# Optimization experiments

Measured on AMD Instinct MI355X. Metric: run time of the kernel, lower is better.

The kernel has to match this reference:

```python
import jax, jax.numpy as jnp
import numpy as np

D = 64      # d_model == initialFeatureSize
H = 8       # n_heads
F2 = D + 2  # hidden_size + 2


def _ln(x, g, b):
    m = x.mean(-1, keepdims=True)
    v = ((x - m) ** 2).mean(-1, keepdims=True)
    return (x - m) / jnp.sqrt(v + 1e-5) * g + b


def _mask_weights(idx):
    # softmax of where(idx>0, 1, -9e15) along axis 1 -> mean over non-pad slots
    return jax.nn.softmax(jnp.where(idx > 0, 1.0, -9e15), axis=1)


def _tblock(x, mask, qkv, Wo, bo, ln, ffW, ffb):
    # standard masked multi-head self-attention block (eval mode, dropout off)
    B, L, Dm = x.shape
    dh = Dm // H
    q = (x @ qkv[0]).reshape(B, L, H, dh)
    k = (x @ qkv[1]).reshape(B, L, H, dh)
    v = (x @ qkv[2]).reshape(B, L, H, dh)
    s = jnp.einsum('blhd,bmhd->bhlm', q, k) / jnp.sqrt(jnp.asarray(dh, x.dtype))
    s = jnp.where(mask[:, None, None, :], -1e9, s)
    ctx = jnp.einsum('bhlm,bmhd->blhd', jax.nn.softmax(s, -1), v).reshape(B, L, Dm)
    x = _ln(x + ctx @ Wo + bo, ln[0, 0], ln[0, 1])
    ff = jax.nn.relu(x @ ffW[0] + ffb[0]) @ ffW[1] + ffb[1]
    return _ln(x + ff, ln[1, 0], ln[1, 1])


def _forward(user_emb, global_cen_emb, local_time_emb, cas_pos_emb, local_inf_emb,
             hgnn_w1, hgnn_w2, hgnn_w3, text_lin_W, text_lin_b,
             weight, weight2, fus_l1_W, fus_l1_b, fus_l2_W, fus_l2_b, out_W, out_b,
             tb_qkv, tb_Wo, tb_bo, tb_ln, tb_ff_W, tb_ff_b,
             text2emb, spread_status,
             data_idx, seq, timestamps, user_level, useq, user_inf, user_cen):
    # --- dead code kept for faithfulness (result unused) ---
    w3n = hgnn_w3 / jnp.linalg.norm(hgnn_w3, axis=1, keepdims=True)
    _tw = (w3n @ w3n.T).mean()
    t = text2emb @ text_lin_W + text_lin_b
    _t = ((t - t.min()) / (t.max() - t.min()) * 999).astype(jnp.int32)
    # --- HGNN layer: gather -> masked mean -> relu -> gather -> masked mean ---
    x = (user_emb + global_cen_emb[user_cen]) @ hgnn_w1            # [N, D]
    edge = jax.nn.relu(jnp.einsum('nlc,nl->nc', x[seq], _mask_weights(seq)))  # [E, D]
    node = jnp.einsum('umc,um->uc', (edge @ hgnn_w2)[useq], _mask_weights(useq))  # [N, D]
    # --- batch gather for attention branches ---
    seq_b = seq[data_idx]                                          # [B, L]
    w_b = _mask_weights(seq_b)
    att_mask = seq_b == 0                                          # PAD == 0
    adj = node[seq_b]                                              # [B, L, D]
    # temporal branch
    h_t = adj + local_time_emb[timestamps[data_idx]]
    o_t = _tblock(h_t, att_mask, tb_qkv[0], tb_Wo[0], tb_bo[0], tb_ln[0], tb_ff_W[0], tb_ff_b[0])
    n_t = jnp.einsum('blc,bl->bc', o_t, w_b)
    n_t = jnp.concatenate([n_t, spread_status[data_idx][:, 2:] / 3600.0 / 24.0], -1) @ weight
    # structural branch
    h_s = adj + local_inf_emb[user_inf[data_idx]] + cas_pos_emb[user_level[data_idx]]
    o_s = _tblock(h_s, att_mask, tb_qkv[1], tb_Wo[1], tb_bo[1], tb_ln[1], tb_ff_W[1], tb_ff_b[1])
    n_s = jnp.einsum('blc,bl->bc', o_s, w_b)
    n_s = jnp.concatenate([n_s, spread_status[data_idx][:, :2]], -1) @ weight2
    # gated fusion
    emb = jnp.stack([n_t, n_s])                                    # [2, B, F2]
    score = jax.nn.softmax(jnp.tanh(emb @ fus_l1_W + fus_l1_b) @ fus_l2_W + fus_l2_b, axis=0)
    fused = (score * emb).sum(0)
    return jax.nn.log_softmax(fused @ out_W + out_b, axis=1)       # [B, 2]


def setup_inputs() -> dict:
    key = jax.random.key(0)
    ks = iter(jax.random.split(key, 48))
    N, E, L, M, B, EMB = 100000, 20000, 50, 20, 1024, 300
    stdv = 1.0 / np.sqrt(D)
    u = lambda shape: jax.random.uniform(next(ks), shape, jnp.float32, -stdv, stdv)
    ri = lambda shape, hi: jax.random.randint(next(ks), shape, 0, hi, jnp.int32)
    ln_init = jnp.broadcast_to(jnp.stack([jnp.ones(D), jnp.zeros(D)])[None, None], (2, 2, 2, D))
    return dict(
        user_emb=u((N, D)), global_cen_emb=u((600, D)), local_time_emb=u((5000, D)),
        cas_pos_emb=u((50, D)), local_inf_emb=u((200, D)),
        hgnn_w1=u((D, D)), hgnn_w2=u((D, D)), hgnn_w3=u((100, EMB)),
        text_lin_W=u((EMB, 200)), text_lin_b=u((200,)),
        weight=u((F2, F2)), weight2=u((F2, F2)),
        fus_l1_W=u((F2, F2)), fus_l1_b=u((F2,)), fus_l2_W=u((F2, 1)), fus_l2_b=u((1,)),
        out_W=u((F2, 2)), out_b=u((2,)),
        tb_qkv=u((2, 3, D, D)), tb_Wo=u((2, D, D)), tb_bo=u((2, D)),
        tb_ln=jnp.array(ln_init),
        tb_ff_W=u((2, 2, D, D)), tb_ff_b=u((2, 2, D)),
        text2emb=jax.random.normal(next(ks), (E, EMB), jnp.float32),
        spread_status=jax.random.uniform(next(ks), (E, 4), jnp.float32, 0.0, 100.0),
        data_idx=ri((B,), E), seq=ri((E, L), N), timestamps=ri((E, L), 5000),
        user_level=ri((E, L), 50), useq=ri((N, M), E), user_inf=ri((E, L), 200),
        user_cen=ri((N,), 600),
    )


def reference(user_emb, global_cen_emb, local_time_emb, cas_pos_emb, local_inf_emb,
              hgnn_w1, hgnn_w2, hgnn_w3, text_lin_W, text_lin_b,
              weight, weight2, fus_l1_W, fus_l1_b, fus_l2_W, fus_l2_b, out_W, out_b,
              tb_qkv, tb_Wo, tb_bo, tb_ln, tb_ff_W, tb_ff_b,
              text2emb, spread_status,
              data_idx, seq, timestamps, user_level, useq, user_inf, user_cen):
    return _forward(user_emb, global_cen_emb, local_time_emb, cas_pos_emb, local_inf_emb,
                    hgnn_w1, hgnn_w2, hgnn_w3, text_lin_W, text_lin_b,
                    weight, weight2, fus_l1_W, fus_l1_b, fus_l2_W, fus_l2_b, out_W, out_b,
                    tb_qkv, tb_Wo, tb_bo, tb_ln, tb_ff_W, tb_ff_b,
                    text2emb, spread_status,
                    data_idx, seq, timestamps, user_level, useq, user_inf, user_cen)
```

## Files before the change

kernel.cpp:

```cpp
#include <hip/hip_runtime.h>
#include <hip/hip_bf16.h>

#define D  64
#define L  50
#define M  20
#define BB 1024
#define F2 66
#define NEDGE 20000
#define NUSER 100000

typedef __attribute__((ext_vector_type(8))) short bf16x8;
typedef __attribute__((ext_vector_type(4))) float f32x4;

#define MFMA(a,b,c) __builtin_amdgcn_mfma_f32_16x16x32_bf16(a,b,c,0,0,0)

__device__ __forceinline__ short f2bf(float f) {
    union { __hip_bfloat16 h; unsigned short u; } cv;
    cv.h = __float2bfloat16(f);
    return (short)cv.u;
}
__device__ __forceinline__ uint32_t pk2(float a, float b) {
    union { __hip_bfloat162 h; uint32_t u; } cv;
    cv.h.x = __float2bfloat16(a);
    cv.h.y = __float2bfloat16(b);
    return cv.u;
}
__device__ __forceinline__ float bf2f(short s) {
    return __uint_as_float(((uint32_t)(unsigned short)s) << 16);
}
__device__ __forceinline__ float bf2fu(unsigned short s) {
    return __uint_as_float(((uint32_t)s) << 16);
}
__device__ __forceinline__ int swz(int row, int col) {
    return row * 64 + (col ^ ((row & 7) << 3));
}
__device__ __forceinline__ float wsum(float v) {
    #pragma unroll
    for (int off = 32; off > 0; off >>= 1) v += __shfl_xor(v, off);
    return v;
}


__global__ __launch_bounds__(256) void k_prep(
    const float* __restrict__ qkv, const float* __restrict__ Wo,
    const float* __restrict__ ffW, const float* __restrict__ w2,
    const float* __restrict__ w1, short* __restrict__ wb)
{
    int idx = blockIdx.x * 256 + threadIdx.x;
    int mat = idx >> 12, e = idx & 4095;
    int c = e >> 6, k = e & 63;
    const float* src;
    if (mat == 13)      src = w1;
    else if (mat == 12) src = w2;
    else {
        int bi = mat / 6, m = mat % 6;
        if (m < 3)       src = qkv + ((size_t)bi * 3 + m) * 4096;
        else if (m == 3) src = Wo + (size_t)bi * 4096;
        else             src = ffW + ((size_t)bi * 2 + (m - 4)) * 4096;
    }
    wb[(size_t)mat * 4096 + c * 64 + k] = f2bf(src[k * 64 + c]);
}


__global__ __launch_bounds__(256) void k_hgnn1m(
    const float* __restrict__ user_emb, const float* __restrict__ cen_emb,
    const int* __restrict__ user_cen, const short* __restrict__ w1t,
    unsigned short* __restrict__ xb)
{
    const int tid = threadIdx.x, lane = tid & 63, lo = lane & 15, hg = lane >> 4, w = tid >> 6;
    const int row0 = blockIdx.x * 64 + 16 * w;
    const int arow = row0 + lo;
    const bool av = arow < NUSER;
    const int cidx = av ? user_cen[arow] : 0;

    f32x4 acc[4];
    #pragma unroll
    for (int c = 0; c < 4; ++c) { acc[c][0] = acc[c][1] = acc[c][2] = acc[c][3] = 0.f; }

    #pragma unroll
    for (int ks = 0; ks < 2; ++ks) {
        bf16x8 a;
        if (av) {
            const float4 u0 = *(const float4*)&user_emb[(size_t)arow * 64 + 32 * ks + 8 * hg];
            const float4 u1 = *(const float4*)&user_emb[(size_t)arow * 64 + 32 * ks + 8 * hg + 4];
            const float4 c0 = *(const float4*)&cen_emb[(size_t)cidx * 64 + 32 * ks + 8 * hg];
            const float4 c1 = *(const float4*)&cen_emb[(size_t)cidx * 64 + 32 * ks + 8 * hg + 4];
            uint32_t p0 = pk2(u0.x + c0.x, u0.y + c0.y);
            uint32_t p1 = pk2(u0.z + c0.z, u0.w + c0.w);
            uint32_t p2 = pk2(u1.x + c1.x, u1.y + c1.y);
            uint32_t p3 = pk2(u1.z + c1.z, u1.w + c1.w);
            union { uint32_t u[4]; bf16x8 v; } af;
            af.u[0] = p0; af.u[1] = p1; af.u[2] = p2; af.u[3] = p3;
            a = af.v;
        } else {
            #pragma unroll
            for (int i = 0; i < 8; ++i) a[i] = 0;
        }
        #pragma unroll
        for (int c = 0; c < 4; ++c) {
            bf16x8 bb = *(const bf16x8*)(w1t + (16 * c + lo) * 64 + 32 * ks + 8 * hg);
            acc[c] = MFMA(a, bb, acc[c]);
        }
    }
    #pragma unroll
    for (int c = 0; c < 4; ++c) {
        #pragma unroll
        for (int r = 0; r < 4; ++r) {
            int row = row0 + 4 * hg + r;
            if (row < NUSER) xb[(size_t)row * 64 + 16 * c + lo] = (unsigned short)f2bf(acc[c][r]);
        }
    }
}


__global__ __launch_bounds__(256) void k_edge_gather(
    const unsigned short* __restrict__ xb, const int* __restrict__ seq,
    unsigned short* __restrict__ em)
{
    const int j = threadIdx.x & 63;
    const int e = blockIdx.x * 4 + (threadIdx.x >> 6);
    int my = (j < L) ? seq[(size_t)e * L + j] : 0;
    int cnt = (int)__popcll(__ballot(j < L && my > 0));
    float wv = cnt ? 1.f / (float)cnt : 1.f / (float)L;
    unsigned short tv[50];
    #pragma unroll
    for (int l = 0; l < 50; ++l) tv[l] = xb[(size_t)__shfl(my, l) * D + j];
    float ss[4] = {0.f, 0.f, 0.f, 0.f};
    #pragma unroll
    for (int l = 0; l < 50; ++l) {
        int idx = __shfl(my, l);
        bool use = cnt ? (idx > 0) : true;
        ss[l & 3] += use ? bf2fu(tv[l]) : 0.f;
    }
    float m = fmaxf(((ss[0] + ss[1]) + (ss[2] + ss[3])) * wv, 0.f);
    em[(size_t)e * D + j] = (unsigned short)f2bf(m);
}


__global__ __launch_bounds__(256) void k_gemm_edge(
    const unsigned short* __restrict__ em, const short* __restrict__ w2t,
    unsigned short* __restrict__ e2b)
{
    const int tid = threadIdx.x, lane = tid & 63, lo = lane & 15, hg = lane >> 4, w = tid >> 6;
    const int row0 = blockIdx.x * 64 + 16 * w;
    bf16x8 zf;
    #pragma unroll
    for (int i = 0; i < 8; ++i) zf[i] = 0;
    f32x4 acc[4];
    #pragma unroll
    for (int c = 0; c < 4; ++c) { acc[c][0] = acc[c][1] = acc[c][2] = acc[c][3] = 0.f; }
    #pragma unroll
    for (int ks = 0; ks < 2; ++ks) {
        bf16x8 a = zf;
        if (row0 + lo < NEDGE)
            a = *(const bf16x8*)&em[(size_t)(row0 + lo) * D + 32 * ks + 8 * hg];
        #pragma unroll
        for (int c = 0; c < 4; ++c) {
            bf16x8 bb = *(const bf16x8*)(w2t + (16 * c + lo) * 64 + 32 * ks + 8 * hg);
            acc[c] = MFMA(a, bb, acc[c]);
        }
    }
    #pragma unroll
    for (int c = 0; c < 4; ++c) {
        #pragma unroll
        for (int r = 0; r < 4; ++r) {
            int row = row0 + 4 * hg + r;
            if (row < NEDGE) e2b[(size_t)row * D + 16 * c + lo] = (unsigned short)f2bf(acc[c][r]);
        }
    }
}


__global__ __launch_bounds__(256) void k_nodem(
    const unsigned short* __restrict__ e2b, const int* __restrict__ seq,
    const int* __restrict__ useq, const int* __restrict__ data_idx,
    unsigned short* __restrict__ nb)
{
    const int j = threadIdx.x & 63;
    const int w = threadIdx.x >> 6;
    const int p = blockIdx.x * 4 + w;
    const int b = p / L, l = p - b * L;
    const int ib = data_idx[b];
    const int u = seq[(size_t)ib * L + l];
    int my = (j < M) ? useq[(size_t)u * M + j] : 0;
    int cnt = (int)__popcll(__ballot(j < M && my > 0));
    float wv = cnt ? 1.f / (float)cnt : 1.f / (float)M;
    unsigned short tv[20];
    #pragma unroll
    for (int m = 0; m < M; ++m) tv[m] = e2b[(size_t)__shfl(my, m) * D + j];
    float ss[4] = {0.f, 0.f, 0.f, 0.f};
    #pragma unroll
    for (int m = 0; m < M; ++m) {
        int q = __shfl(my, m);
        bool use = cnt ? (q > 0) : true;
        ss[m & 3] += use ? bf2fu(tv[m]) : 0.f;
    }
    float acc = ((ss[0] + ss[1]) + (ss[2] + ss[3])) * wv;
    nb[(size_t)p * D + j] = (unsigned short)f2bf(acc);
}

#define XB 0
#define QB 3328
#define KB 6656
#define VBT 9984

__global__ __launch_bounds__(512) void k_tblock2(
    const unsigned short* __restrict__ nb,
    const int* __restrict__ seq, const int* __restrict__ data_idx,
    const int* __restrict__ timestamps, const int* __restrict__ user_inf,
    const int* __restrict__ user_level,
    const float* __restrict__ time_emb, const float* __restrict__ inf_emb,
    const float* __restrict__ pos_emb,
    const short* __restrict__ wb,
    const float* __restrict__ bo_all, const float* __restrict__ ln_all,
    const float* __restrict__ ffb_all, const float* __restrict__ spread,
    const float* __restrict__ weight, const float* __restrict__ weight2,
    float* __restrict__ n_t, float* __restrict__ n_s)
{
    const int tid = threadIdx.x;
    const int lane = tid & 63, lo = lane & 15, hg = lane >> 4, w = tid >> 6;
    const int branch = blockIdx.x & 1, b = blockIdx.x >> 1;
    const int ib = data_idx[b];

    const short* WT  = wb + (size_t)branch * 6 * 4096;
    const float* bo  = bo_all + branch * 64;
    const float* lnp = ln_all + branch * 256;
    const float* ffb = ffb_all + branch * 128;
    const float* Wbr = branch ? weight2 : weight;
    float* nout      = branch ? n_s : n_t;
    const int eoff   = branch ? 0 : 2;
    const float escale = branch ? 1.f : (1.f / 86400.f);

    __shared__ __align__(16) short sm[14080];
    __shared__ float nbuf[4][64];
    __shared__ float nvec[F2];
    __shared__ int   seqi[52];

    for (int i = tid; i < 1600; i += 512) {
        int row = i >> 5, cp = (i & 31) * 2;
        uint32_t nn = *(const uint32_t*)(nb + (size_t)b * 3200 + row * 64 + cp);
        float h0 = bf2fu((unsigned short)(nn & 0xffff));
        float h1 = bf2fu((unsigned short)(nn >> 16));
        if (branch == 0) {
            int ts = timestamps[(size_t)ib * L + row];
            float2 te = *(const float2*)(time_emb + (size_t)ts * 64 + cp);
            h0 += te.x; h1 += te.y;
        } else {
            int inf = user_inf[(size_t)ib * L + row];
            int lev = user_level[(size_t)ib * L + row];
            float2 ie = *(const float2*)(inf_emb + (size_t)inf * 64 + cp);
            float2 pe = *(const float2*)(pos_emb + (size_t)lev * 64 + cp);
            h0 += ie.x + pe.x; h1 += ie.y + pe.y;
        }
        *(uint32_t*)&sm[XB + swz(row, cp)] = pk2(h0, h1);
    }
    if (tid < 52) seqi[tid] = (tid < 50) ? seq[(size_t)ib * L + tid] : 0;
    {
        const int zb0 = XB + 50 * 64, zb1 = QB + 50 * 64, zb2 = KB + 50 * 64;
        for (int i = tid; i < 448; i += 512) {
            ((int*)(sm + zb0))[i] = 0;
            ((int*)(sm + zb1))[i] = 0;
            ((int*)(sm + zb2))[i] = 0;
        }
    }
    __syncthreads();

    #pragma unroll
    for (int t2 = 0; t2 < 2; ++t2) {
        int task = w + 8 * t2;
        if (task < 12) {
            int mat = task >> 2, rt = task & 3;
            f32x4 a4[4];
            #pragma unroll
            for (int c = 0; c < 4; ++c) { a4[c][0] = a4[c][1] = a4[c][2] = a4[c][3] = 0.f; }
            #pragma unroll
            for (int ks = 0; ks < 2; ++ks) {
                bf16x8 xa = *(const bf16x8*)&sm[XB + swz(16 * rt + lo, 32 * ks + 8 * hg)];
                #pragma unroll
                for (int c = 0; c < 4; ++c) {
                    bf16x8 bb = *(const bf16x8*)(WT + (size_t)mat * 4096 +
                                                 (16 * c + lo) * 64 + 32 * ks + 8 * hg);
                    a4[c] = MFMA(xa, bb, a4[c]);
                }
            }
            if (mat == 0) {
                #pragma unroll
                for (int c = 0; c < 4; ++c)
                    #pragma unroll
                    for (int r = 0; r < 4; ++r) {
                        int row = 16 * rt + 4 * hg + r;
                        if (row < 52)
                            sm[QB + swz(row, 16 * c + lo)] = f2bf(a4[c][r] * 0.35355339059327378f);
                    }
            } else if (mat == 1) {
                #pragma unroll
                for (int c = 0; c < 4; ++c)
                    #pragma unroll
                    for (int r = 0; r < 4; ++r) {
                        int row = 16 * rt + 4 * hg + r;
                        if (row < 52) sm[KB + swz(row, 16 * c + lo)] = f2bf(a4[c][r]);
                    }
            } else {
                #pragma unroll
                for (int c = 0; c < 4; ++c)
                    #pragma unroll
                    for (int r = 0; r < 4; ++r) {
                        int row = 16 * rt + 4 * hg + r, col = 16 * c + lo;
                        sm[VBT + swz(col, row)] = (row < 50) ? f2bf(a4[c][r]) : (short)0;
                    }
            }
        }
    }
    __syncthreads();

    int svl = (lane < 50) ? seqi[lane] : 0;
    int cnt = (int)__popcll(__ballot(svl > 0));
    float msel[4][4];
    #pragma unroll
    for (int mt = 0; mt < 4; ++mt) {
        #pragma unroll
        for (int r = 0; r < 4; ++r) {
            int m = 16 * mt + 4 * hg + r;
            msel[mt][r] = (m < 50) ? ((seqi[m] > 0) ? 0.f : -1e9f) : -3.0e38f;
        }
    }

    bf16x8 zf;
    #pragma unroll
    for (int i = 0; i < 8; ++i) zf[i] = 0;

    f32x4 ctx[4];
    {
        int hd = w;
        bf16x8 ka[4], qf[4];
        #pragma unroll
        for (int t = 0; t < 4; ++t) {
            ka[t] = zf; qf[t] = zf;
            if (hg == 0) {
                ka[t] = *(const bf16x8*)&sm[KB + swz(16 * t + lo, hd * 8)];
                qf[t] = *(const bf16x8*)&sm[QB + swz(16 * t + lo, hd * 8)];
            }
        }
        f32x4 s[4][4];
        #pragma unroll
        for (int mt = 0; mt < 4; ++mt) {
            #pragma unroll
            for (int c = 0; c < 4; ++c) {
                f32x4 z; z[0] = z[1] = z[2] = z[3] = 0.f;
                s[mt][c] = MFMA(ka[mt], qf[c], z);
            }
        }
        #pragma unroll
        for (int mt = 0; mt < 4; ++mt) {
            #pragma unroll
            for (int r = 0; r < 4; ++r) {
                float ms = msel[mt][r];
                bool valid = (ms == 0.f);
                #pragma unroll
                for (int c = 0; c < 4; ++c) s[mt][c][r] = valid ? s[mt][c][r] : ms;
            }
        }
        uint32_t pk[4][4][2];
        #pragma unroll
        for (int c = 0; c < 4; ++c) {
            float mx = -3.4e38f;
            #pragma unroll
            for (int mt = 0; mt < 4; ++mt) {
                #pragma unroll
                for (int r = 0; r < 4; ++r) mx = fmaxf(mx, s[mt][c][r]);
            }
            mx = fmaxf(mx, __shfl_xor(mx, 16));
            mx = fmaxf(mx, __shfl_xor(mx, 32));
            float den = 0.f;
            #pragma unroll
            for (int mt = 0; mt < 4; ++mt) {
                #pragma unroll
                for (int r = 0; r < 4; ++r) {
                    float e = __expf(s[mt][c][r] - mx);
                    s[mt][c][r] = e; den += e;
                }
            }
            den += __shfl_xor(den, 16);
            den += __shfl_xor(den, 32);
            float inv = 1.f / den;
            #pragma unroll
            for (int mt = 0; mt < 4; ++mt) {
                pk[mt][c][0] = pk2(s[mt][c][0] * inv, s[mt][c][1] * inv);
                pk[mt][c][1] = pk2(s[mt][c][2] * inv, s[mt][c][3] * inv);
            }
        }
        #pragma unroll
        for (int t = 0; t < 4; ++t) { ctx[t][0] = ctx[t][1] = ctx[t][2] = ctx[t][3] = 0.f; }
        #pragma unroll
        for (int rt = 0; rt < 4; ++rt) {
            #pragma unroll
            for (int ks = 0; ks < 2; ++ks) {
                union { uint32_t u[4]; bf16x8 v; } af;
                #pragma unroll
                for (int j = 0; j < 4; ++j) {
                    int src = lo + 16 * (2 * (hg & 1) + (j >> 1));
                    uint32_t a0 = __shfl(pk[2 * ks][rt][j & 1], src);
                    uint32_t a1 = __shfl(pk[2 * ks + 1][rt][j & 1], src);
                    af.u[j] = (hg < 2) ? a0 : a1;
                }
                bf16x8 bfr = zf;
                if (lo < 8) bfr = *(const bf16x8*)&sm[VBT + swz(hd * 8 + lo, 32 * ks + 8 * hg)];
                ctx[rt] = MFMA(af.v, bfr, ctx[rt]);
            }
        }
    }
    __syncthreads();
    if (lo < 8) {
        #pragma unroll
        for (int rt = 0; rt < 4; ++rt) {
            #pragma unroll
            for (int r = 0; r < 4; ++r) {
                int row = 16 * rt + 4 * hg + r;
                if (row < 52) sm[KB + swz(row, w * 8 + lo)] = f2bf(ctx[rt][r]);
            }
        }
    }
    __syncthreads();

    if (w < 4) {
        float g1[4], b1[4], g2[4], b2[4], boc[4], f1b[4], f2b[4];
        #pragma unroll
        for (int c = 0; c < 4; ++c) {
            int col = 16 * c + lo;
            g1[c] = lnp[col];        b1[c] = lnp[64 + col];
            g2[c] = lnp[128 + col];  b2[c] = lnp[192 + col];
            boc[c] = bo[col]; f1b[c] = ffb[col]; f2b[c] = ffb[64 + col];
        }

        f32x4 acc[4];
        #pragma unroll
        for (int c = 0; c < 4; ++c) { acc[c][0] = acc[c][1] = acc[c][2] = acc[c][3] = 0.f; }
        #pragma unroll
        for (int ks = 0; ks < 2; ++ks) {
            bf16x8 a = *(const bf16x8*)&sm[KB + swz(16 * w + lo, 32 * ks + 8 * hg)];
            #pragma unroll
            for (int c = 0; c < 4; ++c) {
                bf16x8 bb = *(const bf16x8*)(WT + 3 * 4096 + (16 * c + lo) * 64 + 32 * ks + 8 * hg);
                acc[c] = MFMA(a, bb, acc[c]);
            }
        }
        float x1v[4][4];
        #pragma unroll
        for (int r = 0; r < 4; ++r) {
            int row = 16 * w + 4 * hg + r;
            float t0 = bf2f(sm[XB + swz(row, lo)])      + acc[0][r] + boc[0];
            float t1 = bf2f(sm[XB + swz(row, 16 + lo)]) + acc[1][r] + boc[1];
            float t2 = bf2f(sm[XB + swz(row, 32 + lo)]) + acc[2][r] + boc[2];
            float t3 = bf2f(sm[XB + swz(row, 48 + lo)]) + acc[3][r] + boc[3];
            float s1 = t0 + t1 + t2 + t3;
            float q1 = t0 * t0 + t1 * t1 + t2 * t2 + t3 * t3;
            #pragma unroll
            for (int d = 1; d <= 8; d <<= 1) { s1 += __shfl_xor(s1, d); q1 += __shfl_xor(q1, d); }
            float mean = s1 * 0.015625f;
            float var = q1 * 0.015625f - mean * mean;
            float rin = rsqrtf(var + 1e-5f);
            float x0 = (t0 - mean) * rin * g1[0] + b1[0];
            float x1 = (t1 - mean) * rin * g1[1] + b1[1];
            float x2 = (t2 - mean) * rin * g1[2] + b1[2];
            float x3 = (t3 - mean) * rin * g1[3] + b1[3];
            x1v[0][r] = x0; x1v[1][r] = x1; x1v[2][r] = x2; x1v[3][r] = x3;
            if (row < 52) {
                sm[QB + swz(row, lo)]      = f2bf(x0);
                sm[QB + swz(row, 16 + lo)] = f2bf(x1);
                sm[QB + swz(row, 32 + lo)] = f2bf(x2);
                sm[QB + swz(row, 48 + lo)] = f2bf(x3);
            }
        }
        #pragma unroll
        for (int c = 0; c < 4; ++c) { acc[c][0] = acc[c][1] = acc[c][2] = acc[c][3] = 0.f; }
        #pragma unroll
        for (int ks = 0; ks < 2; ++ks) {
            bf16x8 a = *(const bf16x8*)&sm[QB + swz(16 * w + lo, 32 * ks + 8 * hg)];
            #pragma unroll
            for (int c = 0; c < 4; ++c) {
                bf16x8 bb = *(const bf16x8*)(WT + 4 * 4096 + (16 * c + lo) * 64 + 32 * ks + 8 * hg);
                acc[c] = MFMA(a, bb, acc[c]);
            }
        }
        #pragma unroll
        for (int c = 0; c < 4; ++c) {
            #pragma unroll
            for (int r = 0; r < 4; ++r) {
                int row = 16 * w + 4 * hg + r;
                if (row < 52) sm[KB + swz(row, 16 * c + lo)] = f2bf(fmaxf(acc[c][r] + f1b[c], 0.f));
            }
        }
        #pragma unroll
        for (int c = 0; c < 4; ++c) { acc[c][0] = acc[c][1] = acc[c][2] = acc[c][3] = 0.f; }
        #pragma unroll
        for (int ks = 0; ks < 2; ++ks) {
            bf16x8 a = *(const bf16x8*)&sm[KB + swz(16 * w + lo, 32 * ks + 8 * hg)];
            #pragma unroll
            for (int c = 0; c < 4; ++c) {
                bf16x8 bb = *(const bf16x8*)(WT + 5 * 4096 + (16 * c + lo) * 64 + 32 * ks + 8 * hg);
                acc[c] = MFMA(a, bb, acc[c]);
            }
        }
        float wv = (cnt > 0) ? 1.f / (float)cnt : 0.02f;
        float np[4] = {0.f, 0.f, 0.f, 0.f};
        #pragma unroll
        for (int r = 0; r < 4; ++r) {
            int row = 16 * w + 4 * hg + r;
            float t0 = x1v[0][r] + acc[0][r] + f2b[0];
            float t1 = x1v[1][r] + acc[1][r] + f2b[1];
            float t2 = x1v[2][r] + acc[2][r] + f2b[2];
            float t3 = x1v[3][r] + acc[3][r] + f2b[3];
            float s1 = t0 + t1 + t2 + t3;
            float q1 = t0 * t0 + t1 * t1 + t2 * t2 + t3 * t3;
            #pragma unroll
            for (int d = 1; d <= 8; d <<= 1) { s1 += __shfl_xor(s1, d); q1 += __shfl_xor(q1, d); }
            float mean = s1 * 0.015625f;
            float var = q1 * 0.015625f - mean * mean;
            float rin = rsqrtf(var + 1e-5f);
            float wl = 0.f;
            if (row < 50) {
                int sv = seqi[row];
                wl = (cnt > 0) ? ((sv > 0) ? wv : 0.f) : wv;
            }
            np[0] += ((t0 - mean) * rin * g2[0] + b2[0]) * wl;
            np[1] += ((t1 - mean) * rin * g2[1] + b2[1]) * wl;
            np[2] += ((t2 - mean) * rin * g2[2] + b2[2]) * wl;
            np[3] += ((t3 - mean) * rin * g2[3] + b2[3]) * wl;
        }
        #pragma unroll
        for (int c = 0; c < 4; ++c) {
            np[c] += __shfl_xor(np[c], 16);
            np[c] += __shfl_xor(np[c], 32);
        }
        if (hg == 0) {
            #pragma unroll
            for (int c = 0; c < 4; ++c) nbuf[w][16 * c + lo] = np[c];
        }
    }
    __syncthreads();
    if (tid < 64) nvec[tid] = nbuf[0][tid] + nbuf[1][tid] + nbuf[2][tid] + nbuf[3][tid];
    else if (tid == 64) nvec[64] = spread[(size_t)ib * 4 + eoff] * escale;
    else if (tid == 65) nvec[65] = spread[(size_t)ib * 4 + eoff + 1] * escale;
    __syncthreads();
    if (tid < F2) {
        float a = 0.f;
        for (int k = 0; k < F2; ++k) a += nvec[k] * Wbr[k * F2 + tid];
        nout[(size_t)b * F2 + tid] = a;
    }
}


__global__ __launch_bounds__(256) void k_fuse(
    const float* __restrict__ n_t, const float* __restrict__ n_s,
    const float* __restrict__ l1W, const float* __restrict__ l1b,
    const float* __restrict__ l2W, const float* __restrict__ l2b,
    const float* __restrict__ outW, const float* __restrict__ outb,
    float* __restrict__ out)
{
    const int w = threadIdx.x >> 6, j = threadIdx.x & 63;
    const int b = blockIdx.x * 4 + w;
    __shared__ float et[4][F2], es[4][F2], fused[4][F2];
    for (int t = j; t < F2; t += 64) { et[w][t] = n_t[(size_t)b * F2 + t]; es[w][t] = n_s[(size_t)b * F2 + t]; }
    float sl[2];
    for (int s = 0; s < 2; ++s) {
        const float* e = s ? es[w] : et[w];
        float part = 0.f;
        for (int t = j; t < F2; t += 64) {
            float acc = l1b[t];
            for (int k = 0; k < F2; ++k) acc += e[k] * l1W[k * F2 + t];
            part += tanhf(acc) * l2W[t];
        }
        part = wsum(part);
        sl[s] = part + l2b[0];
    }
    float mx = fmaxf(sl[0], sl[1]);
    float e0 = __expf(sl[0] - mx), e1 = __expf(sl[1] - mx);
    float inv = 1.f / (e0 + e1);
    float sc0 = e0 * inv, sc1 = e1 * inv;
    for (int t = j; t < F2; t += 64) fused[w][t] = sc0 * et[w][t] + sc1 * es[w][t];
    float p0 = 0.f, p1 = 0.f;
    for (int t = j; t < F2; t += 64) {
        p0 += fused[w][t] * outW[t * 2 + 0];
        p1 += fused[w][t] * outW[t * 2 + 1];
    }
    p0 = wsum(p0); p1 = wsum(p1);
    if (j == 0) {
        float l0 = p0 + outb[0], l1v = p1 + outb[1];
        float m = fmaxf(l0, l1v);
        float lse = m + logf(__expf(l0 - m) + __expf(l1v - m));
        out[(size_t)b * 2 + 0] = l0 - lse;
        out[(size_t)b * 2 + 1] = l1v - lse;
    }
}

extern "C" void kernel_launch(void* const* d_in, const int* in_sizes, int n_in,
                              void* d_out, int out_size, void* d_ws, size_t ws_size,
                              hipStream_t stream)
{
    (void)in_sizes; (void)n_in; (void)out_size; (void)ws_size;
    const float* user_emb = (const float*)d_in[0];
    const float* cen_emb  = (const float*)d_in[1];
    const float* time_emb = (const float*)d_in[2];
    const float* pos_emb  = (const float*)d_in[3];
    const float* inf_emb  = (const float*)d_in[4];
    const float* w1       = (const float*)d_in[5];
    const float* w2       = (const float*)d_in[6];
    const float* weight   = (const float*)d_in[10];
    const float* weight2  = (const float*)d_in[11];
    const float* l1W      = (const float*)d_in[12];
    const float* l1b      = (const float*)d_in[13];
    const float* l2W      = (const float*)d_in[14];
    const float* l2b      = (const float*)d_in[15];
    const float* outW     = (const float*)d_in[16];
    const float* outb     = (const float*)d_in[17];
    const float* qkv      = (const float*)d_in[18];
    const float* Wo       = (const float*)d_in[19];
    const float* bo       = (const float*)d_in[20];
    const float* lnp      = (const float*)d_in[21];
    const float* ffW      = (const float*)d_in[22];
    const float* ffb      = (const float*)d_in[23];
    const float* spread   = (const float*)d_in[25];
    const int* data_idx   = (const int*)d_in[26];
    const int* seq        = (const int*)d_in[27];
    const int* timestamps = (const int*)d_in[28];
    const int* user_level = (const int*)d_in[29];
    const int* useq       = (const int*)d_in[30];
    const int* user_inf   = (const int*)d_in[31];
    const int* user_cen   = (const int*)d_in[32];

    unsigned short* wbt = (unsigned short*)d_ws;
    unsigned short* xb  = wbt + 57344;
    unsigned short* em  = xb + 6400000;
    unsigned short* e2b = em + 1280000;
    unsigned short* nbm = e2b + 1280000;
    float* n_t = (float*)(nbm + 3276800);
    float* n_s = n_t + 67584;
    float* out = (float*)d_out;

    k_prep<<<224, 256, 0, stream>>>(qkv, Wo, ffW, w2, w1, (short*)wbt);
    k_hgnn1m<<<1563, 256, 0, stream>>>(user_emb, cen_emb, user_cen,
                                       (const short*)wbt + 13 * 4096, xb);
    k_edge_gather<<<5000, 256, 0, stream>>>(xb, seq, em);
    k_gemm_edge<<<313, 256, 0, stream>>>(em, (const short*)wbt + 12 * 4096, e2b);
    k_nodem<<<12800, 256, 0, stream>>>(e2b, seq, useq, data_idx, nbm);
    k_tblock2<<<2048, 512, 0, stream>>>(nbm, seq, data_idx, timestamps, user_inf,
                                        user_level, time_emb, inf_emb, pos_emb,
                                        (const short*)wbt, bo, lnp, ffb, spread,
                                        weight, weight2, n_t, n_s);
    k_fuse<<<256, 256, 0, stream>>>(n_t, n_s, l1W, l1b, l2W, l2b, outW, outb, out);
}
```

Before: 200.3 us.

## Process both transformer branches in one block per batch item

The transformer-block kernel now handles both the time and influence branches for one batch element in a single 512-thread block, not one block per branch. The shared nb row, seq indices and block setup are loaded once, and all 8 waves stay busy in the QKV and FFN stages, where the old per-branch layout left some waves idle. Shared memory per block doubles and each wave holds two context accumulators, which raises register pressure and may reduce occupancy even with the launch-bounds hint.

```diff
diff --git a/kernel.cpp b/kernel.cpp
--- a/kernel.cpp
+++ b/kernel.cpp
@@ -203,8 +203,9 @@
 #define QB 3328
 #define KB 6656
 #define VBT 9984
-
-__global__ __launch_bounds__(512) void k_tblock2(
+#define BRO 14080
+
+__global__ __launch_bounds__(512, 4) void k_tblock2(
     const unsigned short* __restrict__ nb,
     const int* __restrict__ seq, const int* __restrict__ data_idx,
     const int* __restrict__ timestamps, const int* __restrict__ user_inf,
@@ -219,96 +220,86 @@
 {
     const int tid = threadIdx.x;
     const int lane = tid & 63, lo = lane & 15, hg = lane >> 4, w = tid >> 6;
-    const int branch = blockIdx.x & 1, b = blockIdx.x >> 1;
+    const int b = blockIdx.x;
     const int ib = data_idx[b];
 
-    const short* WT  = wb + (size_t)branch * 6 * 4096;
-    const float* bo  = bo_all + branch * 64;
-    const float* lnp = ln_all + branch * 256;
-    const float* ffb = ffb_all + branch * 128;
-    const float* Wbr = branch ? weight2 : weight;
-    float* nout      = branch ? n_s : n_t;
-    const int eoff   = branch ? 0 : 2;
-    const float escale = branch ? 1.f : (1.f / 86400.f);
-
-    __shared__ __align__(16) short sm[14080];
-    __shared__ float nbuf[4][64];
-    __shared__ float nvec[F2];
+    __shared__ __align__(16) short sm[2 * BRO];
+    __shared__ float nbuf[2][4][64];
+    __shared__ float nvec[2][F2];
     __shared__ int   seqi[52];
 
     for (int i = tid; i < 1600; i += 512) {
         int row = i >> 5, cp = (i & 31) * 2;
         uint32_t nn = *(const uint32_t*)(nb + (size_t)b * 3200 + row * 64 + cp);
-        float h0 = bf2fu((unsigned short)(nn & 0xffff));
-        float h1 = bf2fu((unsigned short)(nn >> 16));
-        if (branch == 0) {
-            int ts = timestamps[(size_t)ib * L + row];
-            float2 te = *(const float2*)(time_emb + (size_t)ts * 64 + cp);
-            h0 += te.x; h1 += te.y;
-        } else {
-            int inf = user_inf[(size_t)ib * L + row];
-            int lev = user_level[(size_t)ib * L + row];
-            float2 ie = *(const float2*)(inf_emb + (size_t)inf * 64 + cp);
-            float2 pe = *(const float2*)(pos_emb + (size_t)lev * 64 + cp);
-            h0 += ie.x + pe.x; h1 += ie.y + pe.y;
-        }
-        *(uint32_t*)&sm[XB + swz(row, cp)] = pk2(h0, h1);
+        float n0 = bf2fu((unsigned short)(nn & 0xffff));
+        float n1 = bf2fu((unsigned short)(nn >> 16));
+        int ts  = timestamps[(size_t)ib * L + row];
+        int inf = user_inf[(size_t)ib * L + row];
+        int lev = user_level[(size_t)ib * L + row];
+        float2 te = *(const float2*)(time_emb + (size_t)ts * 64 + cp);
+        float2 ie = *(const float2*)(inf_emb + (size_t)inf * 64 + cp);
+        float2 pe = *(const float2*)(pos_emb + (size_t)lev * 64 + cp);
+        *(uint32_t*)&sm[XB + swz(row, cp)]       = pk2(n0 + te.x, n1 + te.y);
+        *(uint32_t*)&sm[BRO + XB + swz(row, cp)] = pk2(n0 + ie.x + pe.x, n1 + ie.y + pe.y);
     }
     if (tid < 52) seqi[tid] = (tid < 50) ? seq[(size_t)ib * L + tid] : 0;
     {
-        const int zb0 = XB + 50 * 64, zb1 = QB + 50 * 64, zb2 = KB + 50 * 64;
         for (int i = tid; i < 448; i += 512) {
-            ((int*)(sm + zb0))[i] = 0;
-            ((int*)(sm + zb1))[i] = 0;
-            ((int*)(sm + zb2))[i] = 0;
+            ((int*)(sm + XB + 50 * 64))[i] = 0;
+            ((int*)(sm + QB + 50 * 64))[i] = 0;
+            ((int*)(sm + KB + 50 * 64))[i] = 0;
+            ((int*)(sm + BRO + XB + 50 * 64))[i] = 0;
+            ((int*)(sm + BRO + QB + 50 * 64))[i] = 0;
+            ((int*)(sm + BRO + KB + 50 * 64))[i] = 0;
         }
     }
     __syncthreads();
 
     #pragma unroll
-    for (int t2 = 0; t2 < 2; ++t2) {
-        int task = w + 8 * t2;
-        if (task < 12) {
-            int mat = task >> 2, rt = task & 3;
-            f32x4 a4[4];
-            #pragma unroll
-            for (int c = 0; c < 4; ++c) { a4[c][0] = a4[c][1] = a4[c][2] = a4[c][3] = 0.f; }
-            #pragma unroll
-            for (int ks = 0; ks < 2; ++ks) {
-                bf16x8 xa = *(const bf16x8*)&sm[XB + swz(16 * rt + lo, 32 * ks + 8 * hg)];
-                #pragma unroll
-                for (int c = 0; c < 4; ++c) {
-                    bf16x8 bb = *(const bf16x8*)(WT + (size_t)mat * 4096 +
-                                                 (16 * c + lo) * 64 + 32 * ks + 8 * hg);
-                    a4[c] = MFMA(xa, bb, a4[c]);
+    for (int t3 = 0; t3 < 3; ++t3) {
+        int task = w + 8 * t3;
+        int br  = (task >= 12) ? 1 : 0;
+        int rem = task - 12 * br;
+        int mat = rem >> 2, rt = rem & 3;
+        const int RB = br * BRO;
+        const short* WTb = wb + (size_t)br * 6 * 4096 + (size_t)mat * 4096;
+        f32x4 a4[4];
+        #pragma unroll
+        for (int c = 0; c < 4; ++c) { a4[c][0] = a4[c][1] = a4[c][2] = a4[c][3] = 0.f; }
+        #pragma unroll
+        for (int ks = 0; ks < 2; ++ks) {
+            bf16x8 xa = *(const bf16x8*)&sm[RB + XB + swz(16 * rt + lo, 32 * ks + 8 * hg)];
+            #pragma unroll
+            for (int c = 0; c < 4; ++c) {
+                bf16x8 bb = *(const bf16x8*)(WTb + (16 * c + lo) * 64 + 32 * ks + 8 * hg);
+                a4[c] = MFMA(xa, bb, a4[c]);
+            }
+        }
+        if (mat == 0) {
+            #pragma unroll
+            for (int c = 0; c < 4; ++c)
+                #pragma unroll
+                for (int r = 0; r < 4; ++r) {
+                    int row = 16 * rt + 4 * hg + r;
+                    if (row < 52)
+                        sm[RB + QB + swz(row, 16 * c + lo)] = f2bf(a4[c][r] * 0.35355339059327378f);
                 }
-            }
-            if (mat == 0) {
-                #pragma unroll
-                for (int c = 0; c < 4; ++c)
-                    #pragma unroll
-                    for (int r = 0; r < 4; ++r) {
-                        int row = 16 * rt + 4 * hg + r;
-                        if (row < 52)
-                            sm[QB + swz(row, 16 * c + lo)] = f2bf(a4[c][r] * 0.35355339059327378f);
-                    }
-            } else if (mat == 1) {
-                #pragma unroll
-                for (int c = 0; c < 4; ++c)
-                    #pragma unroll
-                    for (int r = 0; r < 4; ++r) {
-                        int row = 16 * rt + 4 * hg + r;
-                        if (row < 52) sm[KB + swz(row, 16 * c + lo)] = f2bf(a4[c][r]);
-                    }
-            } else {
-                #pragma unroll
-                for (int c = 0; c < 4; ++c)
-                    #pragma unroll
-                    for (int r = 0; r < 4; ++r) {
-                        int row = 16 * rt + 4 * hg + r, col = 16 * c + lo;
-                        sm[VBT + swz(col, row)] = (row < 50) ? f2bf(a4[c][r]) : (short)0;
-                    }
-            }
+        } else if (mat == 1) {
+            #pragma unroll
+            for (int c = 0; c < 4; ++c)
+                #pragma unroll
+                for (int r = 0; r < 4; ++r) {
+                    int row = 16 * rt + 4 * hg + r;
+                    if (row < 52) sm[RB + KB + swz(row, 16 * c + lo)] = f2bf(a4[c][r]);
+                }
+        } else {
+            #pragma unroll
+            for (int c = 0; c < 4; ++c)
+                #pragma unroll
+                for (int r = 0; r < 4; ++r) {
+                    int row = 16 * rt + 4 * hg + r, col = 16 * c + lo;
+                    sm[RB + VBT + swz(col, row)] = (row < 50) ? f2bf(a4[c][r]) : (short)0;
+                }
         }
     }
     __syncthreads();
@@ -329,16 +320,18 @@
     #pragma unroll
     for (int i = 0; i < 8; ++i) zf[i] = 0;
 
-    f32x4 ctx[4];
-    {
-        int hd = w;
+    f32x4 ctx2[2][4];
+    const int hd = w;
+    #pragma unroll
+    for (int br = 0; br < 2; ++br) {
+        const int RB = br * BRO;
         bf16x8 ka[4], qf[4];
         #pragma unroll
         for (int t = 0; t < 4; ++t) {
             ka[t] = zf; qf[t] = zf;
             if (hg == 0) {
-                ka[t] = *(const bf16x8*)&sm[KB + swz(16 * t + lo, hd * 8)];
-                qf[t] = *(const bf16x8*)&sm[QB + swz(16 * t + lo, hd * 8)];
+                ka[t] = *(const bf16x8*)&sm[RB + KB + swz(16 * t + lo, hd * 8)];
+                qf[t] = *(const bf16x8*)&sm[RB + QB + swz(16 * t + lo, hd * 8)];
             }
         }
         f32x4 s[4][4];
@@ -390,7 +383,9 @@
             }
         }
         #pragma unroll
-        for (int t = 0; t < 4; ++t) { ctx[t][0] = ctx[t][1] = ctx[t][2] = ctx[t][3] = 0.f; }
+        for (int t = 0; t < 4; ++t) {
+            ctx2[br][t][0] = ctx2[br][t][1] = ctx2[br][t][2] = ctx2[br][t][3] = 0.f;
+        }
         #pragma unroll
         for (int rt = 0; rt < 4; ++rt) {
             #pragma unroll
@@ -404,25 +399,36 @@
                     af.u[j] = (hg < 2) ? a0 : a1;
                 }
                 bf16x8 bfr = zf;
-                if (lo < 8) bfr = *(const bf16x8*)&sm[VBT + swz(hd * 8 + lo, 32 * ks + 8 * hg)];
-                ctx[rt] = MFMA(af.v, bfr, ctx[rt]);
+                if (lo < 8) bfr = *(const bf16x8*)&sm[RB + VBT + swz(hd * 8 + lo, 32 * ks + 8 * hg)];
+                ctx2[br][rt] = MFMA(af.v, bfr, ctx2[br][rt]);
             }
         }
     }
     __syncthreads();
     if (lo < 8) {
         #pragma unroll
-        for (int rt = 0; rt < 4; ++rt) {
-            #pragma unroll
-            for (int r = 0; r < 4; ++r) {
-                int row = 16 * rt + 4 * hg + r;
-                if (row < 52) sm[KB + swz(row, w * 8 + lo)] = f2bf(ctx[rt][r]);
+        for (int br = 0; br < 2; ++br) {
+            const int RB = br * BRO;
+            #pragma unroll
+            for (int rt = 0; rt < 4; ++rt) {
+                #pragma unroll
+                for (int r = 0; r < 4; ++r) {
+                    int row = 16 * rt + 4 * hg + r;
+                    if (row < 52) sm[RB + KB + swz(row, hd * 8 + lo)] = f2bf(ctx2[br][rt][r]);
+                }
             }
         }
     }
     __syncthreads();
 
-    if (w < 4) {
+    {
+        const int ebr = w >> 2, ws = w & 3;
+        const int RB = ebr * BRO;
+        const short* WT  = wb + (size_t)ebr * 6 * 4096;
+        const float* bo  = bo_all + ebr * 64;
+        const float* lnp = ln_all + ebr * 256;
+        const float* ffb = ffb_all + ebr * 128;
+
         float g1[4], b1[4], g2[4], b2[4], boc[4], f1b[4], f2b[4];
         #pragma unroll
         for (int c = 0; c < 4; ++c) {
@@ -437,7 +443,7 @@
         for (int c = 0; c < 4; ++c) { acc[c][0] = acc[c][1] = acc[c][2] = acc[c][3] = 0.f; }
         #pragma unroll
         for (int ks = 0; ks < 2; ++ks) {
-            bf16x8 a = *(const bf16x8*)&sm[KB + swz(16 * w + lo, 32 * ks + 8 * hg)];
+            bf16x8 a = *(const bf16x8*)&sm[RB + KB + swz(16 * ws + lo, 32 * ks + 8 * hg)];
             #pragma unroll
             for (int c = 0; c < 4; ++c) {
                 bf16x8 bb = *(const bf16x8*)(WT + 3 * 4096 + (16 * c + lo) * 64 + 32 * ks + 8 * hg);
@@ -447,11 +453,11 @@
         float x1v[4][4];
         #pragma unroll
         for (int r = 0; r < 4; ++r) {
-            int row = 16 * w + 4 * hg + r;
-            float t0 = bf2f(sm[XB + swz(row, lo)])      + acc[0][r] + boc[0];
-            float t1 = bf2f(sm[XB + swz(row, 16 + lo)]) + acc[1][r] + boc[1];
-            float t2 = bf2f(sm[XB + swz(row, 32 + lo)]) + acc[2][r] + boc[2];
-            float t3 = bf2f(sm[XB + swz(row, 48 + lo)]) + acc[3][r] + boc[3];
+            int row = 16 * ws + 4 * hg + r;
+            float t0 = bf2f(sm[RB + XB + swz(row, lo)])      + acc[0][r] + boc[0];
+            float t1 = bf2f(sm[RB + XB + swz(row, 16 + lo)]) + acc[1][r] + boc[1];
+            float t2 = bf2f(sm[RB + XB + swz(row, 32 + lo)]) + acc[2][r] + boc[2];
+            float t3 = bf2f(sm[RB + XB + swz(row, 48 + lo)]) + acc[3][r] + boc[3];
             float s1 = t0 + t1 + t2 + t3;
             float q1 = t0 * t0 + t1 * t1 + t2 * t2 + t3 * t3;
             #pragma unroll
@@ -465,17 +471,17 @@
             float x3 = (t3 - mean) * rin * g1[3] + b1[3];
             x1v[0][r] = x0; x1v[1][r] = x1; x1v[2][r] = x2; x1v[3][r] = x3;
             if (row < 52) {
-                sm[QB + swz(row, lo)]      = f2bf(x0);
-                sm[QB + swz(row, 16 + lo)] = f2bf(x1);
-                sm[QB + swz(row, 32 + lo)] = f2bf(x2);
-                sm[QB + swz(row, 48 + lo)] = f2bf(x3);
+                sm[RB + QB + swz(row, lo)]      = f2bf(x0);
+                sm[RB + QB + swz(row, 16 + lo)] = f2bf(x1);
+                sm[RB + QB + swz(row, 32 + lo)] = f2bf(x2);
+                sm[RB + QB + swz(row, 48 + lo)] = f2bf(x3);
             }
         }
         #pragma unroll
         for (int c = 0; c < 4; ++c) { acc[c][0] = acc[c][1] = acc[c][2] = acc[c][3] = 0.f; }
         #pragma unroll
         for (int ks = 0; ks < 2; ++ks) {
-            bf16x8 a = *(const bf16x8*)&sm[QB + swz(16 * w + lo, 32 * ks + 8 * hg)];
+            bf16x8 a = *(const bf16x8*)&sm[RB + QB + swz(16 * ws + lo, 32 * ks + 8 * hg)];
             #pragma unroll
             for (int c = 0; c < 4; ++c) {
                 bf16x8 bb = *(const bf16x8*)(WT + 4 * 4096 + (16 * c + lo) * 64 + 32 * ks + 8 * hg);
@@ -486,15 +492,15 @@
         for (int c = 0; c < 4; ++c) {
             #pragma unroll
             for (int r = 0; r < 4; ++r) {
-                int row = 16 * w + 4 * hg + r;
-                if (row < 52) sm[KB + swz(row, 16 * c + lo)] = f2bf(fmaxf(acc[c][r] + f1b[c], 0.f));
+                int row = 16 * ws + 4 * hg + r;
+                if (row < 52) sm[RB + KB + swz(row, 16 * c + lo)] = f2bf(fmaxf(acc[c][r] + f1b[c], 0.f));
             }
         }
         #pragma unroll
         for (int c = 0; c < 4; ++c) { acc[c][0] = acc[c][1] = acc[c][2] = acc[c][3] = 0.f; }
         #pragma unroll
         for (int ks = 0; ks < 2; ++ks) {
-            bf16x8 a = *(const bf16x8*)&sm[KB + swz(16 * w + lo, 32 * ks + 8 * hg)];
+            bf16x8 a = *(const bf16x8*)&sm[RB + KB + swz(16 * ws + lo, 32 * ks + 8 * hg)];
             #pragma unroll
             for (int c = 0; c < 4; ++c) {
                 bf16x8 bb = *(const bf16x8*)(WT + 5 * 4096 + (16 * c + lo) * 64 + 32 * ks + 8 * hg);
@@ -505,7 +511,7 @@
         float np[4] = {0.f, 0.f, 0.f, 0.f};
         #pragma unroll
         for (int r = 0; r < 4; ++r) {
-            int row = 16 * w + 4 * hg + r;
+            int row = 16 * ws + 4 * hg + r;
             float t0 = x1v[0][r] + acc[0][r] + f2b[0];
             float t1 = x1v[1][r] + acc[1][r] + f2b[1];
             float t2 = x1v[2][r] + acc[2][r] + f2b[2];
@@ -534,18 +540,29 @@
         }
         if (hg == 0) {
             #pragma unroll
-            for (int c = 0; c < 4; ++c) nbuf[w][16 * c + lo] = np[c];
+            for (int c = 0; c < 4; ++c) nbuf[ebr][ws][16 * c + lo] = np[c];
         }
     }
     __syncthreads();
-    if (tid < 64) nvec[tid] = nbuf[0][tid] + nbuf[1][tid] + nbuf[2][tid] + nbuf[3][tid];
-    else if (tid == 64) nvec[64] = spread[(size_t)ib * 4 + eoff] * escale;
-    else if (tid == 65) nvec[65] = spread[(size_t)ib * 4 + eoff + 1] * escale;
+    if (tid < 64)
+        nvec[0][tid] = nbuf[0][0][tid] + nbuf[0][1][tid] + nbuf[0][2][tid] + nbuf[0][3][tid];
+    else if (tid < 128)
+        nvec[1][tid - 64] = nbuf[1][0][tid - 64] + nbuf[1][1][tid - 64] +
+                            nbuf[1][2][tid - 64] + nbuf[1][3][tid - 64];
+    else if (tid == 128) nvec[0][64] = spread[(size_t)ib * 4 + 2] * (1.f / 86400.f);
+    else if (tid == 129) nvec[0][65] = spread[(size_t)ib * 4 + 3] * (1.f / 86400.f);
+    else if (tid == 130) nvec[1][64] = spread[(size_t)ib * 4 + 0];
+    else if (tid == 131) nvec[1][65] = spread[(size_t)ib * 4 + 1];
     __syncthreads();
     if (tid < F2) {
         float a = 0.f;
-        for (int k = 0; k < F2; ++k) a += nvec[k] * Wbr[k * F2 + tid];
-        nout[(size_t)b * F2 + tid] = a;
+        for (int k = 0; k < F2; ++k) a += nvec[0][k] * weight[k * F2 + tid];
+        n_t[(size_t)b * F2 + tid] = a;
+    } else if (tid >= 128 && tid < 128 + F2) {
+        int col = tid - 128;
+        float a = 0.f;
+        for (int k = 0; k < F2; ++k) a += nvec[1][k] * weight2[k * F2 + col];
+        n_s[(size_t)b * F2 + col] = a;
     }
 }
 
@@ -643,7 +660,7 @@
     k_edge_gather<<<5000, 256, 0, stream>>>(xb, seq, em);
     k_gemm_edge<<<313, 256, 0, stream>>>(em, (const short*)wbt + 12 * 4096, e2b);
     k_nodem<<<12800, 256, 0, stream>>>(e2b, seq, useq, data_idx, nbm);
-    k_tblock2<<<2048, 512, 0, stream>>>(nbm, seq, data_idx, timestamps, user_inf,
+    k_tblock2<<<1024, 512, 0, stream>>>(nbm, seq, data_idx, timestamps, user_inf,
                                         user_level, time_emb, inf_emb, pos_emb,
                                         (const short*)wbt, bo, lnp, ffb, spread,
                                         weight, weight2, n_t, n_s);
```

New measurement: 188.0 us. -6.1%, faster.
